# Optimization experiments

Measured on AMD Instinct MI355X. Metric: run time of the kernel, lower is better.

## Reference

```python
import jax, jax.numpy as jnp
import numpy as np

B, T, D, HID, H = 256, 256, 72, 512, 1024


def setup_inputs() -> dict:
    key = jax.random.key(0)
    ks = jax.random.split(key, 21)
    s = 0.02
    w = lambda k, sh: jax.random.normal(k, sh, dtype=jnp.float32) * s
    return {
        "x": jax.random.normal(ks[0], (B, T, D), dtype=jnp.float32),
        "to_predict": 10,
        "p2l_w1": w(ks[1], (HID, D)), "p2l_b1": jnp.zeros((HID,), jnp.float32),
        "p2l_w2": w(ks[2], (H, HID)), "p2l_b2": jnp.zeros((H,), jnp.float32),
        "enc_wih": w(ks[3], (3 * H, H)), "enc_whh": w(ks[4], (3 * H, H)),
        "enc_bih": jnp.zeros((3 * H,), jnp.float32), "enc_bhh": jnp.zeros((3 * H,), jnp.float32),
        "dec_wih": w(ks[5], (3 * H, H)), "dec_whh": w(ks[6], (3 * H, H)),
        "dec_bih": jnp.zeros((3 * H,), jnp.float32), "dec_bhh": jnp.zeros((3 * H,), jnp.float32),
        "l2p_w1": w(ks[7], (HID, H)), "l2p_b1": jnp.zeros((HID,), jnp.float32),
        "l2p_w2": w(ks[8], (D, HID)), "l2p_b2": jnp.zeros((D,), jnp.float32),
        "l2s_w1": w(ks[9], (HID, H)), "l2s_b1": jnp.zeros((HID,), jnp.float32),
        "l2s_w2": w(ks[10], (1, HID)), "l2s_b2": jnp.zeros((1,), jnp.float32),
    }


def _lin(x, w, b):
    return x @ w.T + b


def _gru_gates(gi, gh, h):
    # PyTorch gate order: reset, update, new
    i_r, i_z, i_n = jnp.split(gi, 3, axis=-1)
    h_r, h_z, h_n = jnp.split(gh, 3, axis=-1)
    r = jax.nn.sigmoid(i_r + h_r)
    z = jax.nn.sigmoid(i_z + h_z)
    n = jnp.tanh(i_n + r * h_n)
    return (1.0 - z) * n + z * h


def _forward(x, to_predict,
             p2l_w1, p2l_b1, p2l_w2, p2l_b2,
             enc_wih, enc_whh, enc_bih, enc_bhh,
             dec_wih, dec_whh, dec_bih, dec_bhh,
             l2p_w1, l2p_b1, l2p_w2, l2p_b2,
             l2s_w1, l2s_b1, l2s_w2, l2s_b2):
    par2lat = lambda p: jax.nn.relu(_lin(jax.nn.relu(_lin(p, p2l_w1, p2l_b1)), p2l_w2, p2l_b2))
    lat2par = lambda h: _lin(jax.nn.relu(_lin(h, l2p_w1, l2p_b1)), l2p_w2, l2p_b2)

    latent = par2lat(x)  # [B,T,H]
    # encoder GRU (batch_first, single layer, h0 = 0)
    xp = _lin(latent, enc_wih, enc_bih)  # [B,T,3H] precomputed input projections

    def enc_step(h, gi_t):
        h2 = _gru_gates(gi_t, _lin(h, enc_whh, enc_bhh), h)
        return h2, h2

    h0 = jnp.zeros((x.shape[0], H), latent.dtype)
    _, out = jax.lax.scan(enc_step, h0, jnp.swapaxes(xp, 0, 1))
    output = jnp.swapaxes(out, 0, 1)  # [B,T,H]

    # softmax attention pooling over time
    logits = _lin(jax.nn.relu(_lin(output, l2s_w1, l2s_b1)), l2s_w2, l2s_b2)  # [B,T,1]
    weights = jax.nn.softmax(logits, axis=1)
    Rep = jnp.sum(weights * output, axis=1)  # [B,H]

    def dec_step(carry, _):
        hs, p = carry
        inp = par2lat(p)
        hs = _gru_gates(_lin(inp, dec_wih, dec_bih), _lin(hs, dec_whh, dec_bhh), hs)
        pred = lat2par(hs)
        return (hs, pred), pred

    _, preds = jax.lax.scan(dec_step, (Rep, x[:, -1, :]), None, length=to_predict)
    return jnp.transpose(preds, (1, 0, 2)), Rep  # [B,to_predict,72], [B,H]


def reference(x, to_predict,
              p2l_w1, p2l_b1, p2l_w2, p2l_b2,
              enc_wih, enc_whh, enc_bih, enc_bhh,
              dec_wih, dec_whh, dec_bih, dec_bhh,
              l2p_w1, l2p_b1, l2p_w2, l2p_b2,
              l2s_w1, l2s_b1, l2s_w2, l2s_b2):
    return _forward(x, to_predict,
                    p2l_w1, p2l_b1, p2l_w2, p2l_b2,
                    enc_wih, enc_whh, enc_bih, enc_bhh,
                    dec_wih, dec_whh, dec_bih, dec_bhh,
                    l2p_w1, l2p_b1, l2p_w2, l2p_b2,
                    l2s_w1, l2s_b1, l2s_w2, l2s_b2)
```

## Files before the change

### kernel.cpp

```cpp
#include <hip/hip_runtime.h>
#include <hip/hip_bf16.h>
#include <cstdint>
#include <cstddef>


using bf16 = __hip_bfloat16;
typedef __attribute__((ext_vector_type(8))) short short8;
typedef __attribute__((ext_vector_type(4))) short s4_t;
typedef __attribute__((ext_vector_type(4))) float floatx4;

#define B_    256
#define T_    256
#define D_    72
#define DP_   96
#define HID_  512
#define H_    1024
#define H3_   3072
#define NPRED 10
#define CHUNK 32
#define RA    8192

__device__ __forceinline__ float b2f(bf16 v){ return __bfloat162float(v); }
__device__ __forceinline__ bf16  f2b(float v){ return __float2bfloat16(v); }

__device__ __forceinline__ void async_ld16(const bf16* g, bf16* l) {
  __builtin_amdgcn_global_load_lds(
      (const __attribute__((address_space(1))) unsigned int*)g,
      (__attribute__((address_space(3))) unsigned int*)l,
      16, 0, 0);
}

__device__ __forceinline__ short8 load16_cached(const bf16* p) {
  short8 r;
  asm volatile("global_load_dwordx4 %0, %1, off"
               : "=v"(r) : "v"(p) : "memory");
  return r;
}
__device__ __forceinline__ void store8_llc(bf16* p, s4_t v) {
  asm volatile("global_store_dwordx2 %0, %1, off sc0 sc1"
               :: "v"(p), "v"(v) : "memory");
}

enum { EPI_F32 = 0, EPI_BF16 = 1, EPI_BF16_RELU = 2, EPI_BF16_RELU_PERM = 3 };

template<int BM, int BN, int WM, int WN, int EPI>
__global__ __launch_bounds__(256, 2) void gemm_bt(
    const bf16* __restrict__ A, const bf16* __restrict__ B,
    const float* __restrict__ bias, void* __restrict__ Cout,
    int M, int N, int K, int row_off)
{
  constexpr int BK = 32;
  constexpr int NWN = BN / WN;
  constexpr int MT = WM / 16, NT = WN / 16;
  constexpr int ASEG = BM * 4;
  constexpr int TSEG = (BM + BN) * 4;
  static_assert((BM/WM)*(BN/WN) == 4, "4 waves");
  static_assert(TSEG % 256 == 0, "uniform staging");

  __shared__ __align__(16) bf16 smem[(BM + BN) * BK];
  bf16* As = smem;
  bf16* Bs = smem + BM * BK;

  const int tid  = threadIdx.x;
  const int lane = tid & 63;
  const int wave = tid >> 6;
  const int wm = wave / NWN, wn = wave % NWN;
  const int m0 = blockIdx.y * BM, n0 = blockIdx.x * BN;

  floatx4 acc[MT][NT];
#pragma unroll
  for (int i = 0; i < MT; i++)
#pragma unroll
    for (int j = 0; j < NT; j++)
      acc[i][j] = floatx4{0.f, 0.f, 0.f, 0.f};

  const int krow = (lane >> 4) << 3;
  const int r16  = lane & 15;

  for (int k0 = 0; k0 < K; k0 += BK) {
    __syncthreads();
#pragma unroll
    for (int it = 0; it < TSEG / 256; it++) {
      int s = tid + it * 256;
      const bf16* g;
      if (s < ASEG) {
        int row = s >> 2, kseg = s & 3;
        g = A + (size_t)(m0 + row) * K + k0 + kseg * 8;
      } else {
        int s2 = s - ASEG;
        int row = s2 >> 2, kseg = s2 & 3;
        g = B + (size_t)(n0 + row) * K + k0 + kseg * 8;
      }
      async_ld16(g, smem + (size_t)s * 8);
    }
    __syncthreads();
    short8 af[MT], bfr[NT];
#pragma unroll
    for (int i = 0; i < MT; i++)
      af[i] = *(const short8*)(As + (wm * WM + i * 16 + r16) * BK + krow);
#pragma unroll
    for (int j = 0; j < NT; j++)
      bfr[j] = *(const short8*)(Bs + (wn * WN + j * 16 + r16) * BK + krow);
#pragma unroll
    for (int i = 0; i < MT; i++)
#pragma unroll
      for (int j = 0; j < NT; j++)
        acc[i][j] = __builtin_amdgcn_mfma_f32_16x16x32_bf16(af[i], bfr[j], acc[i][j], 0, 0, 0);
  }

#pragma unroll
  for (int i = 0; i < MT; i++) {
#pragma unroll
    for (int j = 0; j < NT; j++) {
      int gn = n0 + wn * WN + j * 16 + r16;
      float bv = bias ? bias[gn] : 0.f;
#pragma unroll
      for (int r = 0; r < 4; r++) {
        int gm = m0 + wm * WM + i * 16 + ((lane >> 4) << 2) + r;
        float v = acc[i][j][r] + bv;
        if (EPI == EPI_BF16_RELU || EPI == EPI_BF16_RELU_PERM) v = fmaxf(v, 0.f);
        size_t orow;
        if (EPI == EPI_BF16_RELU_PERM) {
          int g = row_off + gm;
          orow = (size_t)(g & 255) * 256 + (size_t)(g >> 8);
        } else {
          orow = (size_t)gm;
        }
        if (EPI == EPI_F32) ((float*)Cout)[orow * (size_t)N + gn] = v;
        else                ((bf16*) Cout)[orow * (size_t)N + gn] = f2b(v);
      }
    }
  }
}

__global__ void convert_pad(const float* __restrict__ in, bf16* __restrict__ out,
                            int rows, int kin, int kout)
{
  size_t idx = (size_t)blockIdx.x * blockDim.x + threadIdx.x;
  if (idx >= (size_t)rows * kout) return;
  int r = idx / kout, c = idx % kout;
  out[idx] = (c < kin) ? f2b(in[(size_t)r * kin + c]) : f2b(0.f);
}

__global__ void enc_init(float* __restrict__ h32, unsigned* __restrict__ bar)
{
  int idx = blockIdx.x * blockDim.x + threadIdx.x;
  h32[idx] = 0.f;
  if (idx < 512) bar[idx] = 0u;
}

__global__ void ppad_init(const float* __restrict__ x, bf16* __restrict__ ppad)
{
  int idx = blockIdx.x * blockDim.x + threadIdx.x;
  int b = idx / DP_, c = idx % DP_;
  float v = (c < D_) ? x[((size_t)b * T_ + (T_ - 1)) * D_ + c] : 0.f;
  ppad[idx] = f2b(v);
}

__device__ __forceinline__ float sigm(float v){ return 1.f / (1.f + __expf(-v)); }

#define ENC_SMEM (98304 + 4*64*52*4)
static_assert(ENC_SMEM <= 160*1024, "LDS");

__global__ __launch_bounds__(256, 1) void enc_fused(
    const bf16* __restrict__ xpc_cur,
    const bf16* __restrict__ whh,
    const float* __restrict__ bhh,
    bf16* __restrict__ enc_out,
    float* __restrict__ h32g,
    unsigned* __restrict__ bar,
    int t0,
    const bf16* __restrict__ lat_nxt,
    const bf16* __restrict__ wih,
    const float* __restrict__ bih,
    bf16* __restrict__ xpc_nxt)
{
  extern __shared__ char smem[];
  const int tid  = threadIdx.x;
  const int lane = tid & 63;
  const int wave = tid >> 6;
  const int wg   = blockIdx.x;
  const int r16  = lane & 15;
  const int kq   = lane >> 4;

  if (wg < 128) {
    float* P = (float*)(smem + 98304);
    constexpr int PS = 52;

    const int rgrp = wg >> 5;
    const int rowb = rgrp * 64;
    const int j0   = (wg & 31) * 32;
    const int kb0  = wave * 256;

    unsigned* flagp  = bar + rgrp * 32 + (lane & 31);
    unsigned* myflag = bar + rgrp * 32 + (wg & 31);

    for (int ci = tid; ci < 48 * 128; ci += 256) {
      int wrow = ci >> 7, kslot = ci & 127;
      int g = wrow >> 4, jj = wrow & 15;
      short8 v = *(const short8*)(whh + ((size_t)(g * H_ + j0 + jj)) * H_ + kslot * 8);
      *(short8*)(smem + kslot * 768 + wrow * 16) = v;
    }
    short8 rw[8][3];
#pragma unroll
    for (int it = 0; it < 8; it++)
#pragma unroll
      for (int g = 0; g < 3; g++)
        rw[it][g] = *(const short8*)(whh + ((size_t)(g * H_ + j0 + 16 + r16)) * H_
                                     + kb0 + it * 32 + kq * 8);

    const int row_loc = tid >> 2;
    const int cq      = tid & 3;
    const int b       = rowb + row_loc;
    const int jb0     = j0 + cq * 4;
    const int jb1     = j0 + 16 + cq * 4;

    floatx4 h32r0 = *(const floatx4*)(h32g + (size_t)b * H_ + jb0);
    floatx4 h32r1 = *(const floatx4*)(h32g + (size_t)b * H_ + jb1);
    const floatx4 bhr0 = *(const floatx4*)(bhh + jb0);
    const floatx4 bhz0 = *(const floatx4*)(bhh + H_ + jb0);
    const floatx4 bhn0 = *(const floatx4*)(bhh + 2 * H_ + jb0);
    const floatx4 bhr1 = *(const floatx4*)(bhh + jb1);
    const floatx4 bhz1 = *(const floatx4*)(bhh + H_ + jb1);
    const floatx4 bhn1 = *(const floatx4*)(bhh + 2 * H_ + jb1);

    __syncthreads();

#define ISSUE(IT)                                                              \
    {                                                                          \
      _Pragma("unroll")                                                        \
      for (int rf = 0; rf < 4; rf++)                                           \
        a[(IT) & 3][rf] = load16_cached(hsrc + (size_t)(rowb + rf * 16 + r16) * H_ \
                                        + kb0 + (IT) * 32 + kq * 8);           \
    }
#define GRP(IT, WC)                                                            \
    do {                                                                       \
      const char* bb = smem + (wave * 32 + (IT) * 4 + kq) * 768 + r16 * 16;    \
      short8 bw0 = *(const short8*)(bb);                                       \
      short8 bw1 = *(const short8*)(bb + 256);                                 \
      short8 bw2 = *(const short8*)(bb + 512);                                 \
      asm volatile("s_waitcnt vmcnt(" #WC ")" ::: "memory");                   \
      __builtin_amdgcn_sched_barrier(0);                                       \
      _Pragma("unroll")                                                        \
      for (int rf = 0; rf < 4; rf++) {                                         \
        accA[rf][0] = __builtin_amdgcn_mfma_f32_16x16x32_bf16(a[(IT)&3][rf], bw0, accA[rf][0], 0, 0, 0); \
        accA[rf][1] = __builtin_amdgcn_mfma_f32_16x16x32_bf16(a[(IT)&3][rf], bw1, accA[rf][1], 0, 0, 0); \
        accA[rf][2] = __builtin_amdgcn_mfma_f32_16x16x32_bf16(a[(IT)&3][rf], bw2, accA[rf][2], 0, 0, 0); \
        accB[rf][0] = __builtin_amdgcn_mfma_f32_16x16x32_bf16(a[(IT)&3][rf], rw[IT][0], accB[rf][0], 0, 0, 0); \
        accB[rf][1] = __builtin_amdgcn_mfma_f32_16x16x32_bf16(a[(IT)&3][rf], rw[IT][1], accB[rf][1], 0, 0, 0); \
        accB[rf][2] = __builtin_amdgcn_mfma_f32_16x16x32_bf16(a[(IT)&3][rf], rw[IT][2], accB[rf][2], 0, 0, 0); \
      }                                                                        \
      if ((IT) + 4 < 8) ISSUE((IT) + 4)                                        \
    } while (0)

    for (int ts = 0; ts < CHUNK; ts++) {
      const int tg = t0 + ts;

      const bf16* gi = xpc_cur + ((size_t)ts * B_ + b) * H3_;
      s4_t vr0 = *(const s4_t*)(gi + jb0);
      s4_t vz0 = *(const s4_t*)(gi + H_ + jb0);
      s4_t vn0 = *(const s4_t*)(gi + 2 * H_ + jb0);
      s4_t vr1 = *(const s4_t*)(gi + jb1);
      s4_t vz1 = *(const s4_t*)(gi + H_ + jb1);
      s4_t vn1 = *(const s4_t*)(gi + 2 * H_ + jb1);

      floatx4 accA[4][3], accB[4][3];
#pragma unroll
      for (int rf = 0; rf < 4; rf++)
#pragma unroll
        for (int g = 0; g < 3; g++) {
          accA[rf][g] = floatx4{0.f, 0.f, 0.f, 0.f};
          accB[rf][g] = floatx4{0.f, 0.f, 0.f, 0.f};
        }

      if (tg > 0) {
        const unsigned tgt = (unsigned)tg;
        while (1) {
          unsigned f;
          asm volatile("global_load_dword %0, %1, off sc0 sc1"
                       : "=v"(f) : "v"(flagp) : "memory");
          asm volatile("s_waitcnt vmcnt(0)" ::: "memory");
          if (__all((int)(f >= tgt))) break;
          __builtin_amdgcn_s_sleep(2);
        }
        const bf16* hsrc = enc_out + (size_t)(tg - 1) * B_ * H_;
        short8 a[4][4];
        ISSUE(0) ISSUE(1) ISSUE(2) ISSUE(3)
        GRP(0, 12); GRP(1, 12); GRP(2, 12); GRP(3, 12);
        GRP(4, 12); GRP(5,  8); GRP(6,  4); GRP(7,  0);
      }

#pragma unroll
      for (int rf = 0; rf < 4; rf++)
#pragma unroll
        for (int g = 0; g < 3; g++)
#pragma unroll
          for (int rr = 0; rr < 4; rr++)
            P[(wave * 64 + rf * 16 + kq * 4 + rr) * PS + g * 16 + r16] = accA[rf][g][rr];
      __syncthreads();
      {
        const float* Pr = P + row_loc * PS + cq * 4;
        floatx4 sr4 = floatx4{0.f,0.f,0.f,0.f};
        floatx4 sz4 = floatx4{0.f,0.f,0.f,0.f};
        floatx4 sn4 = floatx4{0.f,0.f,0.f,0.f};
#pragma unroll
        for (int w = 0; w < 4; w++) {
          const float* pp = Pr + w * 64 * PS;
          sr4 += *(const floatx4*)(pp);
          sz4 += *(const floatx4*)(pp + 16);
          sn4 += *(const floatx4*)(pp + 32);
        }
        s4_t outv;
#pragma unroll
        for (int cc = 0; cc < 4; cc++) {
          float xr = __uint_as_float(((unsigned)(unsigned short)vr0[cc]) << 16);
          float xz = __uint_as_float(((unsigned)(unsigned short)vz0[cc]) << 16);
          float xn = __uint_as_float(((unsigned)(unsigned short)vn0[cc]) << 16);
          float rg = sigm(xr + sr4[cc] + bhr0[cc]);
          float zg = sigm(xz + sz4[cc] + bhz0[cc]);
          float ng = tanhf(xn + rg * (sn4[cc] + bhn0[cc]));
          float hnew = (1.f - zg) * ng + zg * h32r0[cc];
          h32r0[cc] = hnew;
          outv[cc] = (short)__builtin_bit_cast(unsigned short, f2b(hnew));
        }
        store8_llc(enc_out + ((size_t)tg * B_ + b) * H_ + jb0, outv);
      }
      __syncthreads();

#pragma unroll
      for (int rf = 0; rf < 4; rf++)
#pragma unroll
        for (int g = 0; g < 3; g++)
#pragma unroll
          for (int rr = 0; rr < 4; rr++)
            P[(wave * 64 + rf * 16 + kq * 4 + rr) * PS + g * 16 + r16] = accB[rf][g][rr];
      __syncthreads();
      {
        const float* Pr = P + row_loc * PS + cq * 4;
        floatx4 sr4 = floatx4{0.f,0.f,0.f,0.f};
        floatx4 sz4 = floatx4{0.f,0.f,0.f,0.f};
        floatx4 sn4 = floatx4{0.f,0.f,0.f,0.f};
#pragma unroll
        for (int w = 0; w < 4; w++) {
          const float* pp = Pr + w * 64 * PS;
          sr4 += *(const floatx4*)(pp);
          sz4 += *(const floatx4*)(pp + 16);
          sn4 += *(const floatx4*)(pp + 32);
        }
        s4_t outv;
#pragma unroll
        for (int cc = 0; cc < 4; cc++) {
          float xr = __uint_as_float(((unsigned)(unsigned short)vr1[cc]) << 16);
          float xz = __uint_as_float(((unsigned)(unsigned short)vz1[cc]) << 16);
          float xn = __uint_as_float(((unsigned)(unsigned short)vn1[cc]) << 16);
          float rg = sigm(xr + sr4[cc] + bhr1[cc]);
          float zg = sigm(xz + sz4[cc] + bhz1[cc]);
          float ng = tanhf(xn + rg * (sn4[cc] + bhn1[cc]));
          float hnew = (1.f - zg) * ng + zg * h32r1[cc];
          h32r1[cc] = hnew;
          outv[cc] = (short)__builtin_bit_cast(unsigned short, f2b(hnew));
        }
        store8_llc(enc_out + ((size_t)tg * B_ + b) * H_ + jb1, outv);
      }

      asm volatile("s_waitcnt vmcnt(0)" ::: "memory");
      __syncthreads();
      if (tid == 0) {
        unsigned v = (unsigned)(tg + 1);
        asm volatile("global_store_dword %0, %1, off sc0 sc1"
                     :: "v"(myflag), "v"(v) : "memory");
      }
    }
#undef GRP
#undef ISSUE

    *(floatx4*)(h32g + (size_t)b * H_ + jb0) = h32r0;
    *(floatx4*)(h32g + (size_t)b * H_ + jb1) = h32r1;

  } else {
    if (xpc_nxt == nullptr) return;
    const int p  = wg - 128;
    const int wm = wave >> 1, wn = wave & 1;
    bf16* As = (bf16*)smem;
    bf16* Bs = As + 128 * 32;
    const int krow = kq << 3;

    for (int tile = 0; tile < 12; tile++) {
      const int t  = p + tile * 128;
      const int m0 = (t / 24) * 128;
      const int n0 = (t % 24) * 128;

      floatx4 acc[4][4];
#pragma unroll
      for (int i = 0; i < 4; i++)
#pragma unroll
        for (int j = 0; j < 4; j++)
          acc[i][j] = floatx4{0.f, 0.f, 0.f, 0.f};

      for (int k0 = 0; k0 < H_; k0 += 32) {
        __syncthreads();
#pragma unroll
        for (int it = 0; it < 4; it++) {
          int s = tid + it * 256;
          const bf16* g;
          if (s < 512) {
            int row = s >> 2, kseg = s & 3;
            g = lat_nxt + (size_t)(m0 + row) * H_ + k0 + kseg * 8;
          } else {
            int s2 = s - 512;
            int row = s2 >> 2, kseg = s2 & 3;
            g = wih + (size_t)(n0 + row) * H_ + k0 + kseg * 8;
          }
          async_ld16(g, (bf16*)smem + (size_t)s * 8);
        }
        __syncthreads();
        short8 af[4], bfr[4];
#pragma unroll
        for (int i = 0; i < 4; i++)
          af[i] = *(const short8*)(As + (wm * 64 + i * 16 + r16) * 32 + krow);
#pragma unroll
        for (int j = 0; j < 4; j++)
          bfr[j] = *(const short8*)(Bs + (wn * 64 + j * 16 + r16) * 32 + krow);
#pragma unroll
        for (int i = 0; i < 4; i++)
#pragma unroll
          for (int j = 0; j < 4; j++)
            acc[i][j] = __builtin_amdgcn_mfma_f32_16x16x32_bf16(af[i], bfr[j], acc[i][j], 0, 0, 0);
      }

#pragma unroll
      for (int i = 0; i < 4; i++)
#pragma unroll
        for (int j = 0; j < 4; j++) {
          int gn = n0 + wn * 64 + j * 16 + r16;
          float bv = bih[gn];
#pragma unroll
          for (int r = 0; r < 4; r++) {
            int gm = m0 + wm * 64 + i * 16 + (kq << 2) + r;
            xpc_nxt[(size_t)gm * H3_ + gn] = f2b(acc[i][j][r] + bv);
          }
        }
      __syncthreads();
    }
  }
}

__global__ void dec_gates(const float* __restrict__ gi, const float* __restrict__ gh,
                          float* __restrict__ hs32, bf16* __restrict__ hs16)
{
  int idx = blockIdx.x * blockDim.x + threadIdx.x;
  int b = idx >> 10, j = idx & (H_ - 1);
  const float* gir = gi + (size_t)b * H3_;
  const float* ghr = gh + (size_t)b * H3_;
  float r = sigm(gir[j] + ghr[j]);
  float z = sigm(gir[j + H_] + ghr[j + H_]);
  float n = tanhf(gir[j + 2 * H_] + r * ghr[j + 2 * H_]);
  float hnew = (1.f - z) * n + z * hs32[idx];
  hs32[idx] = hnew;
  hs16[idx] = f2b(hnew);
}

__global__ void logits_mv(const bf16* __restrict__ ls1, const float* __restrict__ w2,
                          const float* __restrict__ b2, float* __restrict__ logits)
{
  int gw   = (blockIdx.x * blockDim.x + threadIdx.x) >> 6;
  int lane = threadIdx.x & 63;
  const bf16* row = ls1 + (size_t)gw * HID_;
  float s = 0.f;
#pragma unroll
  for (int k = lane; k < HID_; k += 64) s += b2f(row[k]) * w2[k];
#pragma unroll
  for (int off = 32; off > 0; off >>= 1) s += __shfl_down(s, off, 64);
  if (lane == 0) logits[gw] = s + b2[0];
}

__global__ void attention(const float* __restrict__ logits, const bf16* __restrict__ enc_out,
                          float* __restrict__ rep, float* __restrict__ hs32,
                          bf16* __restrict__ hs16)
{
  int b = blockIdx.x, t = threadIdx.x;
  __shared__ float w[T_];
  __shared__ float red[T_];
  float lg = logits[(size_t)t * B_ + b];
  red[t] = lg; __syncthreads();
  for (int s = 128; s > 0; s >>= 1) { if (t < s) red[t] = fmaxf(red[t], red[t + s]); __syncthreads(); }
  float mx = red[0]; __syncthreads();
  float e = __expf(lg - mx);
  w[t] = e; red[t] = e; __syncthreads();
  for (int s = 128; s > 0; s >>= 1) { if (t < s) red[t] += red[t + s]; __syncthreads(); }
  float inv = 1.f / red[0];
  float acc[4] = {0.f, 0.f, 0.f, 0.f};
  for (int tt = 0; tt < T_; tt++) {
    float wt = w[tt] * inv;
    const bf16* row = enc_out + ((size_t)tt * B_ + b) * H_;
#pragma unroll
    for (int i = 0; i < 4; i++) acc[i] += wt * b2f(row[t + i * 256]);
  }
#pragma unroll
  for (int i = 0; i < 4; i++) {
    int j = t + i * 256;
    rep [(size_t)b * H_ + j] = acc[i];
    hs32[(size_t)b * H_ + j] = acc[i];
    hs16[(size_t)b * H_ + j] = f2b(acc[i]);
  }
}

__global__ void pred_k(const bf16* __restrict__ e1, const float* __restrict__ w2,
                       const float* __restrict__ b2, float* __restrict__ out,
                       bf16* __restrict__ ppad, int s)
{
  int b = blockIdx.x, t = threadIdx.x;
  __shared__ float ev[HID_];
  for (int k = t; k < HID_; k += 256) ev[k] = b2f(e1[(size_t)b * HID_ + k]);
  __syncthreads();
  if (t < D_) {
    float acc = b2[t];
    const float* wr = w2 + (size_t)t * HID_;
    for (int k = 0; k < HID_; k++) acc += ev[k] * wr[k];
    out[(size_t)b * (NPRED * D_) + s * D_ + t] = acc;
    ppad[b * DP_ + t] = f2b(acc);
  }
}

extern "C" void kernel_launch(void* const* d_in, const int* in_sizes, int n_in,
                              void* d_out, int out_size, void* d_ws, size_t ws_size,
                              hipStream_t stream)
{
  const float* x       = (const float*)d_in[0];
  const float* p2l_w1  = (const float*)d_in[2];
  const float* p2l_b1  = (const float*)d_in[3];
  const float* p2l_w2  = (const float*)d_in[4];
  const float* p2l_b2  = (const float*)d_in[5];
  const float* enc_wih = (const float*)d_in[6];
  const float* enc_whh = (const float*)d_in[7];
  const float* enc_bih = (const float*)d_in[8];
  const float* enc_bhh = (const float*)d_in[9];
  const float* dec_wih = (const float*)d_in[10];
  const float* dec_whh = (const float*)d_in[11];
  const float* dec_bih = (const float*)d_in[12];
  const float* dec_bhh = (const float*)d_in[13];
  const float* l2p_w1  = (const float*)d_in[14];
  const float* l2p_b1  = (const float*)d_in[15];
  const float* l2p_w2  = (const float*)d_in[16];
  const float* l2p_b2  = (const float*)d_in[17];
  const float* l2s_w1  = (const float*)d_in[18];
  const float* l2s_b1  = (const float*)d_in[19];
  const float* l2s_w2  = (const float*)d_in[20];
  const float* l2s_b2  = (const float*)d_in[21];

  float* out_preds = (float*)d_out;
  float* out_rep   = (float*)d_out + (size_t)B_ * NPRED * D_;

  char* p = (char*)d_ws;
  auto alloc = [&](size_t bytes) -> char* {
    char* r = p; p += (bytes + 255) & ~(size_t)255; return r;
  };
  bf16* w_p2l1 = (bf16*)alloc((size_t)HID_ * DP_ * 2);
  bf16* w_p2l2 = (bf16*)alloc((size_t)H_ * HID_ * 2);
  bf16* w_ewih = (bf16*)alloc((size_t)H3_ * H_ * 2);
  bf16* w_ewhh = (bf16*)alloc((size_t)H3_ * H_ * 2);
  bf16* w_l2p1 = (bf16*)alloc((size_t)HID_ * H_ * 2);
  bf16* w_l2s1 = (bf16*)alloc((size_t)HID_ * H_ * 2);
  bf16* latent = (bf16*)alloc((size_t)B_ * T_ * H_ * 2);
  bf16* xpcA   = (bf16*)alloc((size_t)CHUNK * B_ * H3_ * 2);
  bf16* xpcB   = (bf16*)alloc((size_t)CHUNK * B_ * H3_ * 2);
  float* h32  = (float*)alloc((size_t)B_ * H_ * 4);
  float* hs32 = (float*)alloc((size_t)B_ * H_ * 4);
  bf16*  hs16 = (bf16*) alloc((size_t)B_ * H_ * 2);
  float* logit= (float*)alloc((size_t)B_ * T_ * 4);
  bf16*  d1   = (bf16*) alloc((size_t)B_ * HID_ * 2);
  bf16*  inp  = (bf16*) alloc((size_t)B_ * H_ * 2);
  bf16*  e1   = (bf16*) alloc((size_t)B_ * HID_ * 2);
  bf16*  ppad = (bf16*) alloc((size_t)B_ * DP_ * 2);
  unsigned* bar = (unsigned*)alloc(2048);
  bf16*  enc_out = latent;

  bf16* xb    = xpcB;
  bf16* tmpc  = xpcB + (size_t)B_ * T_ * DP_;
  bf16* lsc   = xpcA;
  float* ghb  = (float*)(xpcA + (size_t)8 * 1024 * 1024);
  float* gib  = ghb + (size_t)B_ * H3_;
  bf16* w_dwih = xpcB;
  bf16* w_dwhh = xpcB + (size_t)H3_ * H_;

  if ((size_t)(p - (char*)d_ws) > ws_size) return;

  const int TB = B_ * T_;

  auto cgrid = [](size_t n) { return dim3((unsigned)((n + 255) / 256)); };
  convert_pad<<<cgrid((size_t)TB * DP_),   256, 0, stream>>>(x,       xb,     TB,   D_,   DP_);
  convert_pad<<<cgrid((size_t)HID_ * DP_), 256, 0, stream>>>(p2l_w1,  w_p2l1, HID_, D_,   DP_);
  convert_pad<<<cgrid((size_t)H_ * HID_),  256, 0, stream>>>(p2l_w2,  w_p2l2, H_,   HID_, HID_);
  convert_pad<<<cgrid((size_t)H3_ * H_),   256, 0, stream>>>(enc_wih, w_ewih, H3_,  H_,   H_);
  convert_pad<<<cgrid((size_t)H3_ * H_),   256, 0, stream>>>(enc_whh, w_ewhh, H3_,  H_,   H_);
  convert_pad<<<cgrid((size_t)HID_ * H_),  256, 0, stream>>>(l2p_w1,  w_l2p1, HID_, H_,   H_);
  convert_pad<<<cgrid((size_t)HID_ * H_),  256, 0, stream>>>(l2s_w1,  w_l2s1, HID_, H_,   H_);

  for (int rc = 0; rc < TB / RA; rc++) {
    { dim3 g(HID_ / 128, RA / 128);
      gemm_bt<128,128,64,64,EPI_BF16_RELU><<<g, 256, 0, stream>>>(
          xb + (size_t)rc * RA * DP_, w_p2l1, p2l_b1, tmpc, RA, HID_, DP_, 0); }
    { dim3 g(H_ / 128, RA / 128);
      gemm_bt<128,128,64,64,EPI_BF16_RELU_PERM><<<g, 256, 0, stream>>>(
          tmpc, w_p2l2, p2l_b2, latent, RA, H_, HID_, rc * RA); }
  }

  (void)hipFuncSetAttribute((const void*)enc_fused,
                            hipFuncAttributeMaxDynamicSharedMemorySize, ENC_SMEM);
  enc_init<<<(B_ * H_) / 256, 256, 0, stream>>>(h32, bar);
  { dim3 g(H3_ / 128, (CHUNK * B_) / 128);
    gemm_bt<128,128,64,64,EPI_BF16><<<g, 256, 0, stream>>>(
        latent, w_ewih, enc_bih, xpcA, CHUNK * B_, H3_, H_, 0); }
  for (int tc = 0; tc < T_ / CHUNK; tc++) {
    bf16* cur = (tc & 1) ? xpcB : xpcA;
    bf16* nxt = (tc < 7) ? ((tc & 1) ? xpcA : xpcB) : nullptr;
    const bf16* latn = latent + (size_t)(tc + 1 < 8 ? tc + 1 : 0) * CHUNK * B_ * H_;
    enc_fused<<<dim3(256), dim3(256), ENC_SMEM, stream>>>(
        cur, w_ewhh, enc_bhh, enc_out, h32, bar, tc * CHUNK,
        latn, w_ewih, enc_bih, nxt);
  }

  for (int rc = 0; rc < TB / RA; rc++) {
    dim3 g(HID_ / 128, RA / 128);
    gemm_bt<128,128,64,64,EPI_BF16_RELU><<<g, 256, 0, stream>>>(
        enc_out + (size_t)rc * RA * H_, w_l2s1, l2s_b1, lsc, RA, HID_, H_, 0);
    logits_mv<<<RA / 4, 256, 0, stream>>>(lsc, l2s_w2, l2s_b2, logit + (size_t)rc * RA);
  }
  attention<<<B_, 256, 0, stream>>>(logit, enc_out, out_rep, hs32, hs16);

  convert_pad<<<cgrid((size_t)H3_ * H_), 256, 0, stream>>>(dec_wih, w_dwih, H3_, H_, H_);
  convert_pad<<<cgrid((size_t)H3_ * H_), 256, 0, stream>>>(dec_whh, w_dwhh, H3_, H_, H_);
  ppad_init<<<(B_ * DP_) / 256, 256, 0, stream>>>(x, ppad);
  for (int s = 0; s < NPRED; s++) {
    { dim3 g(HID_ / 128, B_ / 64);
      gemm_bt<64,128,32,64,EPI_BF16_RELU><<<g, 256, 0, stream>>>(ppad, w_p2l1, p2l_b1, d1, B_, HID_, DP_, 0); }
    { dim3 g(H_ / 128, B_ / 64);
      gemm_bt<64,128,32,64,EPI_BF16_RELU><<<g, 256, 0, stream>>>(d1, w_p2l2, p2l_b2, inp, B_, H_, HID_, 0); }
    { dim3 g(H3_ / 128, B_ / 64);
      gemm_bt<64,128,32,64,EPI_F32><<<g, 256, 0, stream>>>(inp, w_dwih, dec_bih, gib, B_, H3_, H_, 0); }
    { dim3 g(H3_ / 128, B_ / 64);
      gemm_bt<64,128,32,64,EPI_F32><<<g, 256, 0, stream>>>(hs16, w_dwhh, dec_bhh, ghb, B_, H3_, H_, 0); }
    dec_gates<<<(B_ * H_) / 256, 256, 0, stream>>>(gib, ghb, hs32, hs16);
    { dim3 g(HID_ / 128, B_ / 64);
      gemm_bt<64,128,32,64,EPI_BF16_RELU><<<g, 256, 0, stream>>>(hs16, w_l2p1, l2p_b1, e1, B_, HID_, H_, 0); }
    pred_k<<<B_, 256, 0, stream>>>(e1, l2p_w2, l2p_b2, out_preds, ppad, s);
  }
}
```

Baseline: 3.696 ms.

## Fuse score MLP into GEMM epilogue, merge decoder gate GEMMs, tweak flag polling

The attention-score path now uses a new GEMM whose epilogue applies ReLU, takes the dot product with the second-layer weight and writes per-tile partial sums. A small reduction kernel then produces the logits, so the bf16 hidden activation is no longer written and re-read. The two decoder gate GEMMs (input and hidden) run as one launch, selected by the z grid index. The latent chunk size is doubled to halve the number of launches, and the encoder barrier polling now has each wave read its own 8 flags instead of 32 lanes. The final score bias is dropped, which is valid only because softmax is shift-invariant.

Result: faster. 3.242 ms (-12.3%).

```diff
diff --git a/kernel.cpp b/kernel.cpp
--- a/kernel.cpp
+++ b/kernel.cpp
@@ -18,7 +18,7 @@
 #define H3_   3072
 #define NPRED 10
 #define CHUNK 32
-#define RA    8192
+#define RA    16384
 
 __device__ __forceinline__ float b2f(bf16 v){ return __bfloat162float(v); }
 __device__ __forceinline__ bf16  f2b(float v){ return __float2bfloat16(v); }
@@ -133,6 +133,175 @@
   }
 }
 
+__global__ __launch_bounds__(256, 2) void gemm_bt_dual(
+    const bf16* __restrict__ A0, const bf16* __restrict__ B0,
+    const float* __restrict__ bias0, float* __restrict__ C0,
+    const bf16* __restrict__ A1, const bf16* __restrict__ B1,
+    const float* __restrict__ bias1, float* __restrict__ C1,
+    int M, int N, int K)
+{
+  constexpr int BM = 64, BN = 128, BK = 32;
+  constexpr int ASEG = BM * 4, TSEG = (BM + BN) * 4;
+  const bf16* A = blockIdx.z ? A1 : A0;
+  const bf16* B = blockIdx.z ? B1 : B0;
+  const float* bias = blockIdx.z ? bias1 : bias0;
+  float* Cout = blockIdx.z ? C1 : C0;
+
+  __shared__ __align__(16) bf16 smem[(BM + BN) * BK];
+  bf16* As = smem;
+  bf16* Bs = smem + BM * BK;
+
+  const int tid  = threadIdx.x;
+  const int lane = tid & 63;
+  const int wave = tid >> 6;
+  const int wm = wave >> 1, wn = wave & 1;
+  const int m0 = blockIdx.y * BM, n0 = blockIdx.x * BN;
+
+  floatx4 acc[2][4];
+#pragma unroll
+  for (int i = 0; i < 2; i++)
+#pragma unroll
+    for (int j = 0; j < 4; j++)
+      acc[i][j] = floatx4{0.f, 0.f, 0.f, 0.f};
+
+  const int krow = (lane >> 4) << 3;
+  const int r16  = lane & 15;
+
+  for (int k0 = 0; k0 < K; k0 += BK) {
+    __syncthreads();
+#pragma unroll
+    for (int it = 0; it < TSEG / 256; it++) {
+      int s = tid + it * 256;
+      const bf16* g;
+      if (s < ASEG) {
+        int row = s >> 2, kseg = s & 3;
+        g = A + (size_t)(m0 + row) * K + k0 + kseg * 8;
+      } else {
+        int s2 = s - ASEG;
+        int row = s2 >> 2, kseg = s2 & 3;
+        g = B + (size_t)(n0 + row) * K + k0 + kseg * 8;
+      }
+      async_ld16(g, smem + (size_t)s * 8);
+    }
+    __syncthreads();
+    short8 af[2], bfr[4];
+#pragma unroll
+    for (int i = 0; i < 2; i++)
+      af[i] = *(const short8*)(As + (wm * 32 + i * 16 + r16) * BK + krow);
+#pragma unroll
+    for (int j = 0; j < 4; j++)
+      bfr[j] = *(const short8*)(Bs + (wn * 64 + j * 16 + r16) * BK + krow);
+#pragma unroll
+    for (int i = 0; i < 2; i++)
+#pragma unroll
+      for (int j = 0; j < 4; j++)
+        acc[i][j] = __builtin_amdgcn_mfma_f32_16x16x32_bf16(af[i], bfr[j], acc[i][j], 0, 0, 0);
+  }
+
+#pragma unroll
+  for (int i = 0; i < 2; i++)
+#pragma unroll
+    for (int j = 0; j < 4; j++) {
+      int gn = n0 + wn * 64 + j * 16 + r16;
+      float bv = bias[gn];
+#pragma unroll
+      for (int r = 0; r < 4; r++) {
+        int gm = m0 + wm * 32 + i * 16 + ((lane >> 4) << 2) + r;
+        Cout[(size_t)gm * N + gn] = acc[i][j][r] + bv;
+      }
+    }
+}
+
+__global__ __launch_bounds__(256, 2) void score_gemm(
+    const bf16* __restrict__ A,
+    const bf16* __restrict__ Bw,
+    const float* __restrict__ b1,
+    const float* __restrict__ w2,
+    float* __restrict__ part)
+{
+  constexpr int BK = 32;
+  __shared__ __align__(16) bf16 smem[(128 + 128) * BK];
+  __shared__ float pl[128][33];
+  bf16* As = smem;
+  bf16* Bs = smem + 128 * BK;
+
+  const int tid  = threadIdx.x;
+  const int lane = tid & 63;
+  const int wave = tid >> 6;
+  const int wm = wave >> 1, wn = wave & 1;
+  const int m0 = blockIdx.y * 128, n0 = blockIdx.x * 128;
+  const int krow = (lane >> 4) << 3;
+  const int r16  = lane & 15;
+  const int kq   = lane >> 4;
+
+  floatx4 acc[4][4];
+#pragma unroll
+  for (int i = 0; i < 4; i++)
+#pragma unroll
+    for (int j = 0; j < 4; j++)
+      acc[i][j] = floatx4{0.f, 0.f, 0.f, 0.f};
+
+  for (int k0 = 0; k0 < H_; k0 += BK) {
+    __syncthreads();
+#pragma unroll
+    for (int it = 0; it < 4; it++) {
+      int s = tid + it * 256;
+      const bf16* g;
+      if (s < 512) {
+        int row = s >> 2, kseg = s & 3;
+        g = A + (size_t)(m0 + row) * H_ + k0 + kseg * 8;
+      } else {
+        int s2 = s - 512;
+        int row = s2 >> 2, kseg = s2 & 3;
+        g = Bw + (size_t)(n0 + row) * H_ + k0 + kseg * 8;
+      }
+      async_ld16(g, smem + (size_t)s * 8);
+    }
+    __syncthreads();
+    short8 af[4], bfr[4];
+#pragma unroll
+    for (int i = 0; i < 4; i++)
+      af[i] = *(const short8*)(As + (wm * 64 + i * 16 + r16) * BK + krow);
+#pragma unroll
+    for (int j = 0; j < 4; j++)
+      bfr[j] = *(const short8*)(Bs + (wn * 64 + j * 16 + r16) * BK + krow);
+#pragma unroll
+    for (int i = 0; i < 4; i++)
+#pragma unroll
+      for (int j = 0; j < 4; j++)
+        acc[i][j] = __builtin_amdgcn_mfma_f32_16x16x32_bf16(af[i], bfr[j], acc[i][j], 0, 0, 0);
+  }
+
+#pragma unroll
+  for (int i = 0; i < 4; i++) {
+#pragma unroll
+    for (int r = 0; r < 4; r++) {
+      int row = wm * 64 + i * 16 + kq * 4 + r;
+      float s = 0.f;
+#pragma unroll
+      for (int j = 0; j < 4; j++) {
+        int gn = n0 + wn * 64 + j * 16 + r16;
+        s += fmaxf(acc[i][j][r] + b1[gn], 0.f) * w2[gn];
+      }
+      pl[row][wn * 16 + r16] = s;
+    }
+  }
+  __syncthreads();
+  if (tid < 128) {
+    float t = 0.f;
+#pragma unroll
+    for (int c = 0; c < 32; c++) t += pl[tid][c];
+    part[(size_t)(m0 + tid) * 4 + blockIdx.x] = t;
+  }
+}
+
+__global__ void logits_red(const float* __restrict__ part, float* __restrict__ logit)
+{
+  int i = blockIdx.x * blockDim.x + threadIdx.x;
+  logit[i] = part[(size_t)i * 4] + part[(size_t)i * 4 + 1]
+           + part[(size_t)i * 4 + 2] + part[(size_t)i * 4 + 3];
+}
+
 __global__ void convert_pad(const float* __restrict__ in, bf16* __restrict__ out,
                             int rows, int kin, int kout)
 {
@@ -192,7 +361,7 @@
     const int j0   = (wg & 31) * 32;
     const int kb0  = wave * 256;
 
-    unsigned* flagp  = bar + rgrp * 32 + (lane & 31);
+    unsigned* flagp  = bar + rgrp * 32 + wave * 8 + (lane & 7);
     unsigned* myflag = bar + rgrp * 32 + (wg & 31);
 
     for (int ci = tid; ci < 48 * 128; ci += 256) {
@@ -458,20 +627,6 @@
   float hnew = (1.f - z) * n + z * hs32[idx];
   hs32[idx] = hnew;
   hs16[idx] = f2b(hnew);
-}
-
-__global__ void logits_mv(const bf16* __restrict__ ls1, const float* __restrict__ w2,
-                          const float* __restrict__ b2, float* __restrict__ logits)
-{
-  int gw   = (blockIdx.x * blockDim.x + threadIdx.x) >> 6;
-  int lane = threadIdx.x & 63;
-  const bf16* row = ls1 + (size_t)gw * HID_;
-  float s = 0.f;
-#pragma unroll
-  for (int k = lane; k < HID_; k += 64) s += b2f(row[k]) * w2[k];
-#pragma unroll
-  for (int off = 32; off > 0; off >>= 1) s += __shfl_down(s, off, 64);
-  if (lane == 0) logits[gw] = s + b2[0];
 }
 
 __global__ void attention(const float* __restrict__ logits, const bf16* __restrict__ enc_out,
@@ -547,6 +702,7 @@
   const float* l2s_b1  = (const float*)d_in[19];
   const float* l2s_w2  = (const float*)d_in[20];
   const float* l2s_b2  = (const float*)d_in[21];
+  (void)l2s_b2;
 
   float* out_preds = (float*)d_out;
   float* out_rep   = (float*)d_out + (size_t)B_ * NPRED * D_;
@@ -577,7 +733,7 @@
 
   bf16* xb    = xpcB;
   bf16* tmpc  = xpcB + (size_t)B_ * T_ * DP_;
-  bf16* lsc   = xpcA;
+  float* part_g = (float*)xpcB;
   float* ghb  = (float*)(xpcA + (size_t)8 * 1024 * 1024);
   float* gib  = ghb + (size_t)B_ * H3_;
   bf16* w_dwih = xpcB;
@@ -620,12 +776,9 @@
         latn, w_ewih, enc_bih, nxt);
   }
 
-  for (int rc = 0; rc < TB / RA; rc++) {
-    dim3 g(HID_ / 128, RA / 128);
-    gemm_bt<128,128,64,64,EPI_BF16_RELU><<<g, 256, 0, stream>>>(
-        enc_out + (size_t)rc * RA * H_, w_l2s1, l2s_b1, lsc, RA, HID_, H_, 0);
-    logits_mv<<<RA / 4, 256, 0, stream>>>(lsc, l2s_w2, l2s_b2, logit + (size_t)rc * RA);
-  }
+  score_gemm<<<dim3(4, TB / 128), 256, 0, stream>>>(
+      enc_out, w_l2s1, l2s_b1, l2s_w2, part_g);
+  logits_red<<<TB / 256, 256, 0, stream>>>(part_g, logit);
   attention<<<B_, 256, 0, stream>>>(logit, enc_out, out_rep, hs32, hs16);
 
   convert_pad<<<cgrid((size_t)H3_ * H_), 256, 0, stream>>>(dec_wih, w_dwih, H3_, H_, H_);
@@ -636,10 +789,9 @@
       gemm_bt<64,128,32,64,EPI_BF16_RELU><<<g, 256, 0, stream>>>(ppad, w_p2l1, p2l_b1, d1, B_, HID_, DP_, 0); }
     { dim3 g(H_ / 128, B_ / 64);
       gemm_bt<64,128,32,64,EPI_BF16_RELU><<<g, 256, 0, stream>>>(d1, w_p2l2, p2l_b2, inp, B_, H_, HID_, 0); }
-    { dim3 g(H3_ / 128, B_ / 64);
-      gemm_bt<64,128,32,64,EPI_F32><<<g, 256, 0, stream>>>(inp, w_dwih, dec_bih, gib, B_, H3_, H_, 0); }
-    { dim3 g(H3_ / 128, B_ / 64);
-      gemm_bt<64,128,32,64,EPI_F32><<<g, 256, 0, stream>>>(hs16, w_dwhh, dec_bhh, ghb, B_, H3_, H_, 0); }
+    { dim3 g(H3_ / 128, B_ / 64, 2);
+      gemm_bt_dual<<<g, 256, 0, stream>>>(inp, w_dwih, dec_bih, gib,
+                                          hs16, w_dwhh, dec_bhh, ghb, B_, H3_, H_); }
     dec_gates<<<(B_ * H_) / 256, 256, 0, stream>>>(gib, ghb, hs32, hs16);
     { dim3 g(HID_ / 128, B_ / 64);
       gemm_bt<64,128,32,64,EPI_BF16_RELU><<<g, 256, 0, stream>>>(hs16, w_l2p1, l2p_b1, e1, B_, HID_, H_, 0); }
```
